# Kernel optimization log

Hardware: AMD Instinct MI355X
Metric: run time of the kernel (lower is better)

The kernel has to match this reference:

```python
import jax, jax.numpy as jnp
import numpy as np
import math

HIDDEN = 2048
NUM_HEADS = 16
HEAD_DIM = 128
ROPE_BASE = 10000.0


def _rope_emb(seq_len, dim, dtype):
    # freqs[i, j] = i * base**(-2j/dim); emb = concat(freqs, freqs) -> [S, dim]
    inv_freq = 1.0 / (ROPE_BASE ** (jnp.arange(0, dim, 2, dtype=jnp.float32) / dim))
    t = jnp.arange(seq_len, dtype=jnp.float32)
    freqs = t[:, None] * inv_freq[None, :]            # [S, dim/2]
    return jnp.concatenate([freqs, freqs], axis=-1).astype(dtype)  # [S, dim]


def _apply_rope(x, emb):
    # x: [B, H, S, D]; emb: [S, D] broadcast over batch and heads.
    # Roll-based rotary variant from the source: x*cos + roll(x, 1, -1)*sin
    e = emb[None, None, :, :]
    return x * jnp.cos(e) + jnp.roll(x, shift=1, axis=-1) * jnp.sin(e)


def setup_inputs() -> dict:
    key = jax.random.key(0)
    ks = jax.random.split(key, 5)
    B, S = 2, 2048
    scale = 1.0 / math.sqrt(HIDDEN)
    return {
        "hidden_states": jax.random.normal(ks[0], (B, S, HIDDEN), dtype=jnp.float32),
        "Wq": jax.random.normal(ks[1], (HIDDEN, HIDDEN), dtype=jnp.float32) * scale,
        "Wk": jax.random.normal(ks[2], (HIDDEN, HIDDEN), dtype=jnp.float32) * scale,
        "Wv": jax.random.normal(ks[3], (HIDDEN, HIDDEN), dtype=jnp.float32) * scale,
        "Wo": jax.random.normal(ks[4], (HIDDEN, HIDDEN), dtype=jnp.float32) * scale,
    }


def reference(hidden_states, Wq, Wk, Wv, Wo):
    B, S, _ = hidden_states.shape
    H, D = NUM_HEADS, HEAD_DIM

    def split_heads(x):
        return x.reshape(B, S, H, D).transpose(0, 2, 1, 3)  # [B,H,S,D]

    q = split_heads(hidden_states @ Wq)
    k = split_heads(hidden_states @ Wk)
    v = split_heads(hidden_states @ Wv)

    emb = _rope_emb(S, D, hidden_states.dtype)  # [S, D]
    q = _apply_rope(q, emb)
    k = _apply_rope(k, emb)

    scores = jnp.einsum("bhqd,bhkd->bhqk", q, k) / math.sqrt(D)  # [B,H,S,S]
    probs = jax.nn.softmax(scores, axis=-1)
    ctx = jnp.einsum("bhqk,bhkd->bhqd", probs, v)  # [B,H,S,D]
    ctx = ctx.transpose(0, 2, 1, 3).reshape(B, S, H * D)
    return ctx @ Wo
```

## Files before the change

kernel.cpp:

```cpp
#include <hip/hip_runtime.h>

#define HIDDEN 2048
#define SEQ    2048
#define BATCH  2
#define NHEAD  16
#define HDIM   128

typedef __attribute__((ext_vector_type(4))) int    i32x4;
typedef __attribute__((ext_vector_type(4))) float  f32x4;
typedef __attribute__((ext_vector_type(8))) __bf16 bf16x8;

__device__ __forceinline__ unsigned short f2bf(float f) {
    return __builtin_bit_cast(unsigned short, (__bf16)f);
}
__device__ __forceinline__ float bf2f(unsigned short h) {
    unsigned u = ((unsigned)h) << 16;
    return __builtin_bit_cast(float, u);
}
__device__ __forceinline__ void gl_lds16(const unsigned short* g, unsigned short* l) {
    __builtin_amdgcn_global_load_lds(
        (const __attribute__((address_space(1))) unsigned int*)g,
        (__attribute__((address_space(3))) unsigned int*)l, 16, 0, 0);
}

__global__ void k_prep(const float* __restrict__ X, unsigned short* __restrict__ Xb,
                       float* __restrict__ ctab, float* __restrict__ stab,
                       const float* __restrict__ W0, const float* __restrict__ W1,
                       const float* __restrict__ W2, const float* __restrict__ W3,
                       unsigned short* __restrict__ O0, unsigned short* __restrict__ O1,
                       unsigned short* __restrict__ O2, unsigned short* __restrict__ O3)
{
    __shared__ float tile[32][33];
    int bid = blockIdx.x, tid = threadIdx.x;
    if (bid < 16384) {
        int z = bid >> 12, rem = bid & 4095;
        int by = rem >> 6, bx = rem & 63;
        const float* in = (z == 0) ? W0 : (z == 1) ? W1 : (z == 2) ? W2 : W3;
        unsigned short* out = (z == 0) ? O0 : (z == 1) ? O1 : (z == 2) ? O2 : O3;
        float scl = (z == 0) ? 0.12751743f : 1.0f;
        int tx = tid & 31, ty = tid >> 5;
        int x = bx * 32 + tx, y0 = by * 32;
#pragma unroll
        for (int i = 0; i < 4; i++)
            tile[ty + i * 8][tx] = in[(size_t)(y0 + ty + i * 8) * HIDDEN + x];
        __syncthreads();
        int x2 = by * 32 + tx, y2 = bx * 32;
#pragma unroll
        for (int i = 0; i < 4; i++)
            out[(size_t)(y2 + ty + i * 8) * HIDDEN + x2] = f2bf(tile[tx][ty + i * 8] * scl);
    } else if (bid < 24576) {
        int idx = (bid - 16384) * 256 + tid;
        float4 v = ((const float4*)X)[idx];
        ushort4 o;
        o.x = f2bf(v.x); o.y = f2bf(v.y); o.z = f2bf(v.z); o.w = f2bf(v.w);
        ((ushort4*)Xb)[idx] = o;
    } else {
        int idx = (bid - 24576) * 256 + tid;
        int t = idx >> 6, i = idx & 63;
        float inv = expf(-(float)i * 0.14391156831212793f);
        float ang = (float)t * inv;
        ctab[idx] = cosf(ang);
        stab[idx] = sinf(ang);
    }
}

template <int OUTB>
__global__ __launch_bounds__(512, 1) void k_gemm256(
    const unsigned short* __restrict__ A,
    const unsigned short* __restrict__ B0, const unsigned short* __restrict__ B1,
    const unsigned short* __restrict__ B2,
    void* __restrict__ C0, void* __restrict__ C1, void* __restrict__ C2,
    const float* __restrict__ ctab, const float* __restrict__ stab,
    int K)
{
    __shared__ __align__(16) unsigned short S[3 * 24576];
    const int nwg = gridDim.x;
    int id = blockIdx.x;
    int wg = (id & 7) * (nwg >> 3) + (id >> 3);
    const int z = wg >> 8;
    const int my = (wg >> 4) & 15, nx = wg & 15;
    const unsigned short* Bm = (z == 0) ? B0 : (z == 1 ? B1 : B2);
    void* Cv = (z == 0) ? C0 : (z == 1 ? C1 : C2);
    const int m0 = my * 256, n0 = nx * 128;
    const int tid = threadIdx.x, l = tid & 63, w = tid >> 6;
    const int wm = w >> 1, wn = w & 1;
    const int lr = l & 15, lg = l >> 4;

    const unsigned short* sg[6];
    int so[6];
#pragma unroll
    for (int j = 0; j < 4; j++) {
        int c = tid + j * 512, row = c >> 3, k8 = c & 7;
        sg[j] = A + (size_t)(m0 + row) * K + ((k8 ^ (row & 7)) * 8);
        so[j] = row * 64 + k8 * 8;
    }
#pragma unroll
    for (int j = 0; j < 2; j++) {
        int c = tid + j * 512, row = c >> 3, k8 = c & 7;
        sg[4 + j] = Bm + (size_t)(n0 + row) * K + ((k8 ^ (row & 7)) * 8);
        so[4 + j] = 16384 + row * 64 + k8 * 8;
    }

    f32x4 acc[4][4] = {};

    auto stage = [&](int t) {
        unsigned short* buf = &S[(t % 3) * 24576];
        const int ko = t * 64;
#pragma unroll
        for (int j = 0; j < 6; j++) gl_lds16(sg[j] + ko, &buf[so[j]]);
    };
    auto compute = [&](int t) {
        const unsigned short* buf = &S[(t % 3) * 24576];
        const unsigned short* bb = buf + 16384;
        const int xk0 = (lg ^ (lr & 7)) * 8, xk1 = ((4 + lg) ^ (lr & 7)) * 8;
        i32x4 af0[4], af1[4], bf0[4], bf1[4];
#pragma unroll
        for (int i = 0; i < 4; i++) {
            int R = (wm * 64 + i * 16 + lr) * 64;
            af0[i] = *(const i32x4*)&buf[R + xk0];
            af1[i] = *(const i32x4*)&buf[R + xk1];
        }
#pragma unroll
        for (int j = 0; j < 4; j++) {
            int R = (wn * 64 + j * 16 + lr) * 64;
            bf0[j] = *(const i32x4*)&bb[R + xk0];
            bf1[j] = *(const i32x4*)&bb[R + xk1];
        }
        __builtin_amdgcn_s_setprio(1);
#pragma unroll
        for (int i = 0; i < 4; i++)
#pragma unroll
            for (int j = 0; j < 4; j++)
                acc[i][j] = __builtin_amdgcn_mfma_f32_16x16x32_bf16(
                    __builtin_bit_cast(bf16x8, af0[i]),
                    __builtin_bit_cast(bf16x8, bf0[j]), acc[i][j], 0, 0, 0);
#pragma unroll
        for (int i = 0; i < 4; i++)
#pragma unroll
            for (int j = 0; j < 4; j++)
                acc[i][j] = __builtin_amdgcn_mfma_f32_16x16x32_bf16(
                    __builtin_bit_cast(bf16x8, af1[i]),
                    __builtin_bit_cast(bf16x8, bf1[j]), acc[i][j], 0, 0, 0);
        __builtin_amdgcn_s_setprio(0);
    };

    const int nt = K / 64;
    stage(0); stage(1);
    for (int t = 0; t < nt - 1; ++t) {
        asm volatile("s_waitcnt vmcnt(6)" ::: "memory");
        __builtin_amdgcn_s_barrier();
        __builtin_amdgcn_sched_barrier(0);
        if (t < nt - 2) stage(t + 2);
        compute(t);
    }
    asm volatile("s_waitcnt vmcnt(0)" ::: "memory");
    __builtin_amdgcn_s_barrier();
    __builtin_amdgcn_sched_barrier(0);
    compute(nt - 1);

    if (OUTB && z == 2) {
        unsigned short* Vt = (unsigned short*)Cv;
        const int bb_ = m0 >> 11;
        const int tb = (m0 & 2047) + wm * 64;
#pragma unroll
        for (int i = 0; i < 4; i++)
#pragma unroll
            for (int j = 0; j < 4; j++) {
                int t0 = tb + i * 16 + lg * 4;
                int n = n0 + wn * 64 + j * 16 + lr;
                ushort4 pk;
                pk.x = f2bf(acc[i][j][0]); pk.y = f2bf(acc[i][j][1]);
                pk.z = f2bf(acc[i][j][2]); pk.w = f2bf(acc[i][j][3]);
                *(ushort4*)&Vt[((size_t)(bb_ * 2048 + n)) * 2048 + t0] = pk;
            }
    } else if (OUTB) {
        float* xch = (float*)S;
        if (lr == 15) {
#pragma unroll
            for (int i = 0; i < 4; i++)
#pragma unroll
                for (int r = 0; r < 4; r++)
                    xch[(((wm << 1) | wn) * 4 + i) * 16 + lg * 4 + r] = acc[i][3][r];
        }
        __syncthreads();
        unsigned short* Co = (unsigned short*)Cv;
#pragma unroll
        for (int i = 0; i < 4; i++)
#pragma unroll
            for (int r = 0; r < 4; r++) {
                int m = m0 + wm * 64 + i * 16 + lg * 4 + r;
                int t = m & 2047;
                float ldsprev = xch[(((wm << 1) | (wn ^ 1)) * 4 + i) * 16 + lg * 4 + r];
#pragma unroll
                for (int j = 0; j < 4; j++) {
                    float v = acc[i][j][r];
                    float pA = __shfl(v, l - 1);
                    float prev;
                    if (j == 0) {
                        prev = (lr == 0) ? ldsprev : pA;
                    } else {
                        float pB = __shfl(acc[i][j - 1][r], (l & 48) + 15);
                        prev = (lr == 0) ? pB : pA;
                    }
                    float cc = ctab[t * 64 + j * 16 + lr];
                    float ss = stab[t * 64 + j * 16 + lr];
                    int n = n0 + wn * 64 + j * 16 + lr;
                    Co[(size_t)m * 2048 + n] = f2bf(v * cc + prev * ss);
                }
            }
    } else {
#pragma unroll
        for (int i = 0; i < 4; i++)
#pragma unroll
            for (int j = 0; j < 4; j++)
#pragma unroll
                for (int r = 0; r < 4; r++) {
                    int m = m0 + wm * 64 + i * 16 + lg * 4 + r;
                    int n = n0 + wn * 64 + j * 16 + lr;
                    ((float*)Cv)[(size_t)m * 2048 + n] = acc[i][j][r];
                }
    }
}

__global__ __launch_bounds__(512) void k_attn(
    const unsigned short* __restrict__ Q, const unsigned short* __restrict__ K,
    const unsigned short* __restrict__ Vt, unsigned short* __restrict__ ctx)
{
    __shared__ __align__(16) unsigned short Klds[3][64 * 128];
    __shared__ __align__(16) unsigned short Vlds[3][128 * 64];
    __shared__ __align__(16) unsigned short Plds[8][32 * 64];
    const int tid = threadIdx.x, l = tid & 63, w = tid >> 6;
    const int lr = l & 15, lg = l >> 4;
    const int bid = blockIdx.x;
    const int sX = bid >> 3;
    const int bh = (bid & 7) * 4 + (sX >> 3);
    const int q0 = (sX & 7) * 256;
    const int b = bh >> 4, h = bh & 15;

    i32x4 qf[2][4];
#pragma unroll
    for (int qh = 0; qh < 2; qh++) {
        const unsigned short* qbase =
            Q + (size_t)(b * SEQ + q0 + w * 32 + qh * 16 + lr) * HIDDEN + h * HDIM + lg * 8;
#pragma unroll
        for (int c = 0; c < 4; c++) qf[qh][c] = *(const i32x4*)(qbase + c * 32);
    }

    const unsigned short* kg[2];
    const unsigned short* vg[2];
    int kl[2], vl[2];
#pragma unroll
    for (int c = 0; c < 2; c++) {
        int cc = tid + c * 512;
        {   int row = cc >> 4, ch = cc & 15, sch = ch ^ (row & 7);
            kg[c] = K + (size_t)(b * SEQ + row) * HIDDEN + h * HDIM + sch * 8;
            kl[c] = cc * 8; }
        {   int row = cc >> 3, ch = cc & 7, sch = ch ^ (row & 7);
            vg[c] = Vt + (size_t)(bh * HDIM + row) * SEQ + sch * 8;
            vl[c] = cc * 8; }
    }

    auto stage = [&](int t) {
        const int bsel = t % 3;
        const size_t ko = (size_t)t * 64;
#pragma unroll
        for (int c = 0; c < 2; c++) {
            gl_lds16(kg[c] + ko * HIDDEN, &Klds[bsel][kl[c]]);
            gl_lds16(vg[c] + ko,          &Vlds[bsel][vl[c]]);
        }
    };

    f32x4 acc[2][8] = {};
    float m_run[2] = {-1e30f, -1e30f}, l_run[2] = {0.f, 0.f};

    stage(0); stage(1);
    const int nt = SEQ / 64;
    for (int t = 0; t < nt; ++t) {
        if (t + 1 < nt) { asm volatile("s_waitcnt vmcnt(4)" ::: "memory"); }
        else            { asm volatile("s_waitcnt vmcnt(0)" ::: "memory"); }
        __builtin_amdgcn_s_barrier();
        __builtin_amdgcn_sched_barrier(0);
        if (t + 2 < nt) stage(t + 2);
        const unsigned short* Kb_ = Klds[t % 3];
        const unsigned short* Vb_ = Vlds[t % 3];

        f32x4 s[4][2];
        __builtin_amdgcn_s_setprio(1);
#pragma unroll
        for (int ks = 0; ks < 4; ks++) {
            s[ks][0] = f32x4{0.f, 0.f, 0.f, 0.f};
            s[ks][1] = f32x4{0.f, 0.f, 0.f, 0.f};
#pragma unroll
            for (int c = 0; c < 4; c++) {
                i32x4 kf = *(const i32x4*)&Kb_[(ks * 16 + lr) * 128 + ((c * 4 + lg) ^ (lr & 7)) * 8];
                s[ks][0] = __builtin_amdgcn_mfma_f32_16x16x32_bf16(
                    __builtin_bit_cast(bf16x8, kf), __builtin_bit_cast(bf16x8, qf[0][c]),
                    s[ks][0], 0, 0, 0);
                s[ks][1] = __builtin_amdgcn_mfma_f32_16x16x32_bf16(
                    __builtin_bit_cast(bf16x8, kf), __builtin_bit_cast(bf16x8, qf[1][c]),
                    s[ks][1], 0, 0, 0);
            }
        }
        __builtin_amdgcn_s_setprio(0);

        float p[2][4][4];
        float fac[2];
        bool need_any = false;
#pragma unroll
        for (int qh = 0; qh < 2; qh++) {
            float mx0 = fmaxf(fmaxf(s[0][qh][0], s[0][qh][1]), fmaxf(s[0][qh][2], s[0][qh][3]));
            float mx1 = fmaxf(fmaxf(s[1][qh][0], s[1][qh][1]), fmaxf(s[1][qh][2], s[1][qh][3]));
            float mx2 = fmaxf(fmaxf(s[2][qh][0], s[2][qh][1]), fmaxf(s[2][qh][2], s[2][qh][3]));
            float mx3 = fmaxf(fmaxf(s[3][qh][0], s[3][qh][1]), fmaxf(s[3][qh][2], s[3][qh][3]));
            float pmax = fmaxf(fmaxf(mx0, mx1), fmaxf(mx2, mx3));
            pmax = fmaxf(pmax, __shfl_xor(pmax, 16));
            pmax = fmaxf(pmax, __shfl_xor(pmax, 32));
            bool need = pmax > m_run[qh] + 8.0f;
            fac[qh] = need ? __builtin_amdgcn_exp2f(m_run[qh] - pmax) : 1.0f;
            float mn = need ? pmax : m_run[qh];
            m_run[qh] = mn;
            float psum = 0.f;
#pragma unroll
            for (int ks = 0; ks < 4; ks++) {
                float e0 = __builtin_amdgcn_exp2f(s[ks][qh][0] - mn);
                float e1 = __builtin_amdgcn_exp2f(s[ks][qh][1] - mn);
                float e2 = __builtin_amdgcn_exp2f(s[ks][qh][2] - mn);
                float e3 = __builtin_amdgcn_exp2f(s[ks][qh][3] - mn);
                p[qh][ks][0] = e0; p[qh][ks][1] = e1;
                p[qh][ks][2] = e2; p[qh][ks][3] = e3;
                psum += (e0 + e1) + (e2 + e3);
            }
            psum += __shfl_xor(psum, 16);
            psum += __shfl_xor(psum, 32);
            l_run[qh] = l_run[qh] * fac[qh] + psum;
            need_any |= need;
        }

        unsigned short* pw = &Plds[w][0];
#pragma unroll
        for (int qh = 0; qh < 2; qh++)
#pragma unroll
            for (int ks = 0; ks < 4; ks++) {
                ushort4 pk;
                pk.x = f2bf(p[qh][ks][0]); pk.y = f2bf(p[qh][ks][1]);
                pk.z = f2bf(p[qh][ks][2]); pk.w = f2bf(p[qh][ks][3]);
                int chunk = ks * 2 + (lg >> 1);
                *(ushort4*)&pw[(qh * 16 + lr) * 64 + ((chunk ^ (lr & 7)) * 8) + (lg & 1) * 4] = pk;
            }

        if (__any((int)need_any)) {
#pragma unroll
            for (int qh = 0; qh < 2; qh++) {
                float facq[4];
#pragma unroll
                for (int r = 0; r < 4; r++) facq[r] = __shfl(fac[qh], lg * 4 + r);
#pragma unroll
                for (int db = 0; db < 8; db++)
#pragma unroll
                    for (int r = 0; r < 4; r++) acc[qh][db][r] *= facq[r];
            }
        }

        __builtin_amdgcn_s_setprio(1);
#pragma unroll
        for (int kk = 0; kk < 2; kk++) {
            i32x4 pf0 = *(const i32x4*)&pw[(lr) * 64 + ((kk * 4 + lg) ^ (lr & 7)) * 8];
            i32x4 pf1 = *(const i32x4*)&pw[(16 + lr) * 64 + ((kk * 4 + lg) ^ (lr & 7)) * 8];
#pragma unroll
            for (int db = 0; db < 8; db++) {
                i32x4 vf = *(const i32x4*)&Vb_[(db * 16 + lr) * 64 + ((kk * 4 + lg) ^ (lr & 7)) * 8];
                acc[0][db] = __builtin_amdgcn_mfma_f32_16x16x32_bf16(
                    __builtin_bit_cast(bf16x8, pf0), __builtin_bit_cast(bf16x8, vf),
                    acc[0][db], 0, 0, 0);
                acc[1][db] = __builtin_amdgcn_mfma_f32_16x16x32_bf16(
                    __builtin_bit_cast(bf16x8, pf1), __builtin_bit_cast(bf16x8, vf),
                    acc[1][db], 0, 0, 0);
            }
        }
        __builtin_amdgcn_s_setprio(0);
    }

#pragma unroll
    for (int qh = 0; qh < 2; qh++) {
        float inv[4];
#pragma unroll
        for (int r = 0; r < 4; r++) inv[r] = 1.0f / __shfl(l_run[qh], lg * 4 + r);
#pragma unroll
        for (int db = 0; db < 8; db++)
#pragma unroll
            for (int r = 0; r < 4; r++) {
                int trow = q0 + w * 32 + qh * 16 + lg * 4 + r;
                ctx[(size_t)(b * SEQ + trow) * HIDDEN + h * HDIM + db * 16 + lr] =
                    f2bf(acc[qh][db][r] * inv[r]);
            }
    }
}

extern "C" void kernel_launch(void* const* d_in, const int* in_sizes, int n_in,
                              void* d_out, int out_size, void* d_ws, size_t ws_size,
                              hipStream_t stream)
{
    (void)in_sizes; (void)n_in; (void)out_size; (void)ws_size;
    const float* X  = (const float*)d_in[0];
    const float* Wq = (const float*)d_in[1];
    const float* Wk = (const float*)d_in[2];
    const float* Wv = (const float*)d_in[3];
    const float* Wo = (const float*)d_in[4];
    float* out = (float*)d_out;
    char* ws = (char*)d_ws;

    unsigned short* Xb  = (unsigned short*)(ws);
    unsigned short* WqT = (unsigned short*)(ws + 16777216);
    unsigned short* WkT = (unsigned short*)(ws + 25165824);
    unsigned short* WvT = (unsigned short*)(ws + 33554432);
    unsigned short* WoT = (unsigned short*)(ws + 41943040);
    unsigned short* Qb  = (unsigned short*)(ws + 50331648);
    unsigned short* Kb  = (unsigned short*)(ws + 67108864);
    unsigned short* Vt  = (unsigned short*)(ws + 100663296);
    unsigned short* Cx  = (unsigned short*)(ws + 117440512);
    float* ctab = (float*)(ws + 134217728);
    float* stab = (float*)(ws + 134742016);

    k_prep<<<25088, 256, 0, stream>>>(X, Xb, ctab, stab, Wq, Wk, Wv, Wo,
                                      WqT, WkT, WvT, WoT);
    k_gemm256<1><<<768, 512, 0, stream>>>(Xb, WqT, WkT, WvT, Qb, Kb, Vt,
                                          ctab, stab, 2048);
    k_attn<<<256, 512, 0, stream>>>(Qb, Kb, Vt, Cx);
    k_gemm256<0><<<256, 512, 0, stream>>>(Cx, WoT, WoT, WoT, out, out, out,
                                          nullptr, nullptr, 2048);
}
```

Before: 259.3 us.

## Halve GEMM K-tile to 32 so two workgroups fit per CU

Cuts the GEMM K-step from 64 to 32, halving the triple-buffered LDS footprint to 72 KB, and raises launch bounds to two 512-thread workgroups per CU. Staging drops the XOR swizzle and uses 64-byte rows, and the loop waits on vmcnt(3) with a final vmcnt(0) instead of a peeled tail. The aim is higher occupancy so one workgroup's memory waits can hide behind the other's MFMA work. In exchange it doubles the barrier and loop count per K, and unswizzled 64-byte rows may cause LDS bank conflicts. It also tightens the per-thread register budget, which could spill the 64 accumulator registers.

```diff
diff --git a/kernel.cpp b/kernel.cpp
--- a/kernel.cpp
+++ b/kernel.cpp
@@ -65,7 +65,7 @@
 }
 
 template <int OUTB>
-__global__ __launch_bounds__(512, 1) void k_gemm256(
+__global__ __launch_bounds__(512, 2) void k_gemm256(
     const unsigned short* __restrict__ A,
     const unsigned short* __restrict__ B0, const unsigned short* __restrict__ B1,
     const unsigned short* __restrict__ B2,
@@ -73,7 +73,7 @@
     const float* __restrict__ ctab, const float* __restrict__ stab,
     int K)
 {
-    __shared__ __align__(16) unsigned short S[3 * 24576];
+    __shared__ __align__(16) unsigned short S[3 * 12288];
     const int nwg = gridDim.x;
     int id = blockIdx.x;
     int wg = (id & 7) * (nwg >> 3) + (id >> 3);
@@ -86,77 +86,59 @@
     const int wm = w >> 1, wn = w & 1;
     const int lr = l & 15, lg = l >> 4;
 
-    const unsigned short* sg[6];
-    int so[6];
-#pragma unroll
-    for (int j = 0; j < 4; j++) {
-        int c = tid + j * 512, row = c >> 3, k8 = c & 7;
-        sg[j] = A + (size_t)(m0 + row) * K + ((k8 ^ (row & 7)) * 8);
-        so[j] = row * 64 + k8 * 8;
-    }
+    const unsigned short* sg[3];
+    int so[3];
 #pragma unroll
     for (int j = 0; j < 2; j++) {
-        int c = tid + j * 512, row = c >> 3, k8 = c & 7;
-        sg[4 + j] = Bm + (size_t)(n0 + row) * K + ((k8 ^ (row & 7)) * 8);
-        so[4 + j] = 16384 + row * 64 + k8 * 8;
+        int c = tid + j * 512, row = c >> 2, k8 = c & 3;
+        sg[j] = A + (size_t)(m0 + row) * K + k8 * 8;
+        so[j] = row * 32 + k8 * 8;
+    }
+    {
+        int c = tid, row = c >> 2, k8 = c & 3;
+        sg[2] = Bm + (size_t)(n0 + row) * K + k8 * 8;
+        so[2] = 8192 + row * 32 + k8 * 8;
     }
 
     f32x4 acc[4][4] = {};
 
     auto stage = [&](int t) {
-        unsigned short* buf = &S[(t % 3) * 24576];
-        const int ko = t * 64;
-#pragma unroll
-        for (int j = 0; j < 6; j++) gl_lds16(sg[j] + ko, &buf[so[j]]);
+        unsigned short* buf = &S[(t % 3) * 12288];
+        const int ko = t * 32;
+#pragma unroll
+        for (int j = 0; j < 3; j++) gl_lds16(sg[j] + ko, &buf[so[j]]);
     };
     auto compute = [&](int t) {
-        const unsigned short* buf = &S[(t % 3) * 24576];
-        const unsigned short* bb = buf + 16384;
-        const int xk0 = (lg ^ (lr & 7)) * 8, xk1 = ((4 + lg) ^ (lr & 7)) * 8;
-        i32x4 af0[4], af1[4], bf0[4], bf1[4];
-#pragma unroll
-        for (int i = 0; i < 4; i++) {
-            int R = (wm * 64 + i * 16 + lr) * 64;
-            af0[i] = *(const i32x4*)&buf[R + xk0];
-            af1[i] = *(const i32x4*)&buf[R + xk1];
-        }
-#pragma unroll
-        for (int j = 0; j < 4; j++) {
-            int R = (wn * 64 + j * 16 + lr) * 64;
-            bf0[j] = *(const i32x4*)&bb[R + xk0];
-            bf1[j] = *(const i32x4*)&bb[R + xk1];
-        }
+        const unsigned short* buf = &S[(t % 3) * 12288];
+        const unsigned short* bb = buf + 8192;
+        i32x4 af[4], bfr[4];
+#pragma unroll
+        for (int i = 0; i < 4; i++)
+            af[i] = *(const i32x4*)&buf[(wm * 64 + i * 16 + lr) * 32 + lg * 8];
+#pragma unroll
+        for (int j = 0; j < 4; j++)
+            bfr[j] = *(const i32x4*)&bb[(wn * 64 + j * 16 + lr) * 32 + lg * 8];
         __builtin_amdgcn_s_setprio(1);
 #pragma unroll
         for (int i = 0; i < 4; i++)
 #pragma unroll
             for (int j = 0; j < 4; j++)
                 acc[i][j] = __builtin_amdgcn_mfma_f32_16x16x32_bf16(
-                    __builtin_bit_cast(bf16x8, af0[i]),
-                    __builtin_bit_cast(bf16x8, bf0[j]), acc[i][j], 0, 0, 0);
-#pragma unroll
-        for (int i = 0; i < 4; i++)
-#pragma unroll
-            for (int j = 0; j < 4; j++)
-                acc[i][j] = __builtin_amdgcn_mfma_f32_16x16x32_bf16(
-                    __builtin_bit_cast(bf16x8, af1[i]),
-                    __builtin_bit_cast(bf16x8, bf1[j]), acc[i][j], 0, 0, 0);
+                    __builtin_bit_cast(bf16x8, af[i]),
+                    __builtin_bit_cast(bf16x8, bfr[j]), acc[i][j], 0, 0, 0);
         __builtin_amdgcn_s_setprio(0);
     };
 
-    const int nt = K / 64;
+    const int nt = K / 32;
     stage(0); stage(1);
-    for (int t = 0; t < nt - 1; ++t) {
-        asm volatile("s_waitcnt vmcnt(6)" ::: "memory");
+    for (int t = 0; t < nt; ++t) {
+        if (t + 1 < nt) { asm volatile("s_waitcnt vmcnt(3)" ::: "memory"); }
+        else            { asm volatile("s_waitcnt vmcnt(0)" ::: "memory"); }
         __builtin_amdgcn_s_barrier();
         __builtin_amdgcn_sched_barrier(0);
-        if (t < nt - 2) stage(t + 2);
+        if (t + 2 < nt) stage(t + 2);
         compute(t);
     }
-    asm volatile("s_waitcnt vmcnt(0)" ::: "memory");
-    __builtin_amdgcn_s_barrier();
-    __builtin_amdgcn_sched_barrier(0);
-    compute(nt - 1);
 
     if (OUTB && z == 2) {
         unsigned short* Vt = (unsigned short*)Cv;
```

Measured after the change: 268.6 us. 1.04x slower.
